# Optimization experiments

Hardware: AMD Instinct MI355X
Metric: run time of the kernel (lower is better)

Reference implementation:

```python
import jax, jax.numpy as jnp
import numpy as np

N_NODES = 100000
N_EDGES = 3200000
D = 64
NEG_SLOPE = 0.01  # torch F.leaky_relu default


def setup_inputs() -> dict:
    key = jax.random.key(0)
    ks = jax.random.split(key, 7)
    s = 1.0 / np.sqrt(D)
    x = jax.random.normal(ks[0], (N_NODES, D), jnp.float32)
    src = jax.random.randint(ks[1], (N_EDGES,), 0, N_NODES)
    dst = jax.random.randint(ks[2], (N_EDGES,), 0, N_NODES)
    W1a = jax.random.normal(ks[3], (D, D), jnp.float32) * s
    W2a = jax.random.normal(ks[4], (D, D), jnp.float32) * s
    W1b = jax.random.normal(ks[5], (D, D), jnp.float32) * s
    W2b = jax.random.normal(ks[6], (D, D), jnp.float32) * s
    return {"x": x, "W1a": W1a, "W2a": W2a, "W1b": W1b, "W2b": W2b,
            "src": src, "dst": dst}


def _ngcf_conv(x, src, dst, norm, W1, W2):
    # message: norm_ij * (W1 x_j + W2 (x_j (*) x_i)), aggregated at dst i,
    # plus self-transform W1 x_i  (NGCF propagation rule, pre-activation)
    xs = x[src]            # [E, D] gather of neighbor feats
    xd = x[dst]            # [E, D] gather of center feats
    msg = norm[:, None] * (xs @ W1 + (xs * xd) @ W2)   # [E, D]
    agg = jax.ops.segment_sum(msg, dst, num_segments=x.shape[0])
    return x @ W1 + agg


def reference(x, W1a, W2a, W1b, W2b, src, dst):
    n = x.shape[0]
    ones = jnp.ones(src.shape[0], x.dtype)
    deg = jnp.maximum(jax.ops.segment_sum(ones, dst, num_segments=n), 1.0)
    norm = jax.lax.rsqrt(deg[src] * deg[dst])          # 1/sqrt(d_j d_i)
    h1 = jax.nn.leaky_relu(_ngcf_conv(x, src, dst, norm, W1a, W2a), NEG_SLOPE)
    h2 = jax.nn.leaky_relu(_ngcf_conv(h1, src, dst, norm, W1b, W2b), NEG_SLOPE)
    h3 = _ngcf_conv(h2, src, dst, norm, W1b, W2b)      # no activation (matches source)
    return jnp.concatenate([h1, h2, h3], axis=-1)      # [N, 3*D]
```

## Files before the change

### kernel.cpp

```cpp
#include <hip/hip_runtime.h>
#include <hip/hip_bf16.h>

#define N_NODES 100000
#define N_EDGES 3200000
#define D 64
#define NEG_SLOPE 0.01f

#define B_SHIFT 9
#define NB ((N_NODES + 511) >> B_SHIFT)
#define T_EDGES 4096
#define NBIN ((N_EDGES + T_EDGES - 1) / T_EDGES)

__device__ __forceinline__ unsigned short f2bf(float f) {
    __hip_bfloat16 h = __float2bfloat16(f);
    return *reinterpret_cast<unsigned short*>(&h);
}
__device__ __forceinline__ float bflo(unsigned int u) { return __uint_as_float(u << 16); }
__device__ __forceinline__ float bfhi(unsigned int u) { return __uint_as_float(u & 0xffff0000u); }

__global__ __launch_bounds__(256) void bhist_k(const int* __restrict__ dst, int* __restrict__ btot) {
    __shared__ int hist[NB];
    int tid = threadIdx.x;
    for (int b = tid; b < NB; b += 256) hist[b] = 0;
    __syncthreads();
    int e0 = blockIdx.x * T_EDGES;
    int e1 = min(e0 + T_EDGES, N_EDGES);
    for (int e = e0 + tid; e < e1; e += 256) atomicAdd(&hist[dst[e] >> B_SHIFT], 1);
    __syncthreads();
    for (int b = tid; b < NB; b += 256) {
        int h = hist[b];
        if (h) atomicAdd(&btot[b], h);
    }
}

__global__ __launch_bounds__(256) void bscan_k(const int* __restrict__ btot, int* __restrict__ bbase) {
    __shared__ int wsum[4];
    int t = threadIdx.x;
    int lane = t & 63, w = t >> 6;
    int v = (t < NB) ? btot[t] : 0;
    int incl = v;
    #pragma unroll
    for (int o = 1; o < 64; o <<= 1) {
        int u = __shfl_up(incl, o, 64);
        if (lane >= o) incl += u;
    }
    if (lane == 63) wsum[w] = incl;
    __syncthreads();
    int woff = 0;
    for (int k = 0; k < w; ++k) woff += wsum[k];
    if (t < NB) bbase[t] = woff + incl - v;
    if (t == NB) bbase[NB] = N_EDGES;
}

__global__ __launch_bounds__(256) void bucket_k(const int* __restrict__ src, const int* __restrict__ dst,
                                                const int* __restrict__ bbase, int* __restrict__ bcnt2,
                                                int2* __restrict__ pairs) {
    __shared__ int hist[NB];
    __shared__ int lbase[NB];
    __shared__ int lcnt[NB];
    __shared__ int gbase[NB];
    __shared__ int wsum[4];
    __shared__ int2 buf[T_EDGES];
    int tid = threadIdx.x;
    for (int b = tid; b < NB; b += 256) { hist[b] = 0; lcnt[b] = 0; }
    __syncthreads();
    int e0 = blockIdx.x * T_EDGES;
    int e1 = min(e0 + T_EDGES, N_EDGES);
    for (int e = e0 + tid; e < e1; e += 256) atomicAdd(&hist[dst[e] >> B_SHIFT], 1);
    __syncthreads();
    {
        int v = (tid < NB) ? hist[tid] : 0;
        int lane = tid & 63, w = tid >> 6;
        int incl = v;
        #pragma unroll
        for (int o = 1; o < 64; o <<= 1) {
            int u = __shfl_up(incl, o, 64);
            if (lane >= o) incl += u;
        }
        if (lane == 63) wsum[w] = incl;
        __syncthreads();
        int woff = 0;
        for (int k = 0; k < w; ++k) woff += wsum[k];
        if (tid < NB) {
            int excl = woff + incl - v;
            lbase[tid] = excl;
            int p = v ? atomicAdd(&bcnt2[tid], v) : 0;
            gbase[tid] = bbase[tid] + p - excl;
        }
    }
    __syncthreads();
    for (int e = e0 + tid; e < e1; e += 256) {
        int sv = src[e], dv = dst[e];
        int b = dv >> B_SHIFT;
        int loc = lbase[b] + atomicAdd(&lcnt[b], 1);
        buf[loc] = make_int2(sv, dv);
    }
    __syncthreads();
    int n = e1 - e0;
    for (int i = tid; i < n; i += 256) {
        int2 pr = buf[i];
        int b = pr.y >> B_SHIFT;
        pairs[gbase[b] + i] = pr;
    }
}

__global__ __launch_bounds__(512) void fine_k(const int2* __restrict__ pairs, const int* __restrict__ bbase,
                                              int* __restrict__ degi, int* __restrict__ offs,
                                              float* __restrict__ rsd, int* __restrict__ csr_src) {
    __shared__ int cnt[512];
    __shared__ int offl[512];
    __shared__ int wsum[8];
    int b = blockIdx.x, t = threadIdx.x;
    int start = bbase[b];
    int end = bbase[b + 1];
    cnt[t] = 0;
    __syncthreads();
    for (int e = start + t; e < end; e += 512) atomicAdd(&cnt[pairs[e].y & 511], 1);
    __syncthreads();
    int d = cnt[t];
    int lane = t & 63, w = t >> 6;
    int incl = d;
    #pragma unroll
    for (int o = 1; o < 64; o <<= 1) {
        int u = __shfl_up(incl, o, 64);
        if (lane >= o) incl += u;
    }
    if (lane == 63) wsum[w] = incl;
    __syncthreads();
    int woff = 0;
    for (int k = 0; k < w; ++k) woff += wsum[k];
    int myoff = start + woff + incl - d;
    offl[t] = myoff;
    int n = (b << B_SHIFT) + t;
    if (n < N_NODES) {
        degi[n] = d;
        offs[n] = myoff;
        rsd[n] = rsqrtf((float)(d > 0 ? d : 1));
    }
    cnt[t] = 0;
    __syncthreads();
    for (int e = start + t; e < end; e += 512) {
        int2 pr = pairs[e];
        int li = pr.y & 511;
        int p = atomicAdd(&cnt[li], 1);
        csr_src[offl[li] + p] = pr.x;
    }
}

__global__ __launch_bounds__(256) void cvt_k(const float* __restrict__ x, const float* __restrict__ rsd,
                                             unsigned short* __restrict__ xb) {
    int i = blockIdx.x * 256 + threadIdx.x;
    if (i < N_NODES * 16) {
        int node = i >> 4;
        float rn = rsd[node];
        float4 v = ((const float4*)x)[i];
        unsigned int lo = ((unsigned int)f2bf(rn * v.y) << 16) | f2bf(rn * v.x);
        unsigned int hi = ((unsigned int)f2bf(rn * v.w) << 16) | f2bf(rn * v.z);
        ((uint2*)xb)[i] = make_uint2(lo, hi);
    }
}

__global__ __launch_bounds__(256) void agg_k(const unsigned short* __restrict__ xb,
                                             const float* __restrict__ rsd,
                                             const int* __restrict__ offs, const int* __restrict__ degi,
                                             const int* __restrict__ csr_src, float* __restrict__ s) {
    int node = blockIdx.x * 4 + (threadIdx.x >> 6);
    if (node >= N_NODES) return;
    int lane = threadIdx.x & 63;
    int g = lane >> 3;
    int q = lane & 7;
    int start = offs[node];
    int deg = degi[node];
    const uint4* in4 = (const uint4*)xb;
    float acc0 = 0.f, acc1 = 0.f, acc2 = 0.f, acc3 = 0.f;
    float acc4 = 0.f, acc5 = 0.f, acc6 = 0.f, acc7 = 0.f;
    for (int base = 0; base < deg; base += 64) {
        int m = min(deg - base, 64);
        int idxv = csr_src[start + base + min(lane, m - 1)];
        for (int j = 0; j < m; j += 32) {
            int e0 = j + g, e1 = j + 8 + g, e2 = j + 16 + g, e3 = j + 24 + g;
            bool v0 = e0 < m, v1 = e1 < m, v2 = e2 < m, v3 = e3 < m;
            int s0 = __shfl(idxv, e0, 64);
            int s1 = __shfl(idxv, v1 ? e1 : 0, 64);
            int s2 = __shfl(idxv, v2 ? e2 : 0, 64);
            int s3 = __shfl(idxv, v3 ? e3 : 0, 64);
            uint4 p0 = in4[(size_t)s0 * 8 + q];
            uint4 p1 = in4[(size_t)s1 * 8 + q];
            uint4 p2 = in4[(size_t)s2 * 8 + q];
            uint4 p3 = in4[(size_t)s3 * 8 + q];
            float w0 = v0 ? 1.f : 0.f, w1 = v1 ? 1.f : 0.f;
            float w2 = v2 ? 1.f : 0.f, w3 = v3 ? 1.f : 0.f;
            acc0 += w0 * bflo(p0.x); acc1 += w0 * bfhi(p0.x);
            acc2 += w0 * bflo(p0.y); acc3 += w0 * bfhi(p0.y);
            acc4 += w0 * bflo(p0.z); acc5 += w0 * bfhi(p0.z);
            acc6 += w0 * bflo(p0.w); acc7 += w0 * bfhi(p0.w);
            acc0 += w1 * bflo(p1.x); acc1 += w1 * bfhi(p1.x);
            acc2 += w1 * bflo(p1.y); acc3 += w1 * bfhi(p1.y);
            acc4 += w1 * bflo(p1.z); acc5 += w1 * bfhi(p1.z);
            acc6 += w1 * bflo(p1.w); acc7 += w1 * bfhi(p1.w);
            acc0 += w2 * bflo(p2.x); acc1 += w2 * bfhi(p2.x);
            acc2 += w2 * bflo(p2.y); acc3 += w2 * bfhi(p2.y);
            acc4 += w2 * bflo(p2.z); acc5 += w2 * bfhi(p2.z);
            acc6 += w2 * bflo(p2.w); acc7 += w2 * bfhi(p2.w);
            acc0 += w3 * bflo(p3.x); acc1 += w3 * bfhi(p3.x);
            acc2 += w3 * bflo(p3.y); acc3 += w3 * bfhi(p3.y);
            acc4 += w3 * bflo(p3.z); acc5 += w3 * bfhi(p3.z);
            acc6 += w3 * bflo(p3.w); acc7 += w3 * bfhi(p3.w);
        }
    }
    #pragma unroll
    for (int off = 8; off < 64; off <<= 1) {
        acc0 += __shfl_xor(acc0, off, 64); acc1 += __shfl_xor(acc1, off, 64);
        acc2 += __shfl_xor(acc2, off, 64); acc3 += __shfl_xor(acc3, off, 64);
        acc4 += __shfl_xor(acc4, off, 64); acc5 += __shfl_xor(acc5, off, 64);
        acc6 += __shfl_xor(acc6, off, 64); acc7 += __shfl_xor(acc7, off, 64);
    }
    if (g == 0) {
        float rn = rsd[node];
        float4 r0, r1;
        r0.x = rn * acc0; r0.y = rn * acc1; r0.z = rn * acc2; r0.w = rn * acc3;
        r1.x = rn * acc4; r1.y = rn * acc5; r1.z = rn * acc6; r1.w = rn * acc7;
        ((float4*)s)[node * 16 + q * 2]     = r0;
        ((float4*)s)[node * 16 + q * 2 + 1] = r1;
    }
}

__global__ __launch_bounds__(256) void comb_k(const float* __restrict__ in, int stride,
                                              const float* __restrict__ s,
                                              const float* __restrict__ W1, const float* __restrict__ W2,
                                              float* __restrict__ out, int act,
                                              unsigned short* __restrict__ hb, const float* __restrict__ rsd,
                                              int bfout) {
    __shared__ float W1s[D * D];
    __shared__ float W2s[D * D];
    __shared__ float aL[4][4][D];
    __shared__ float bL[4][4][D];
    int tid = threadIdx.x;
    {
        const float4* w1v = (const float4*)W1;
        const float4* w2v = (const float4*)W2;
        float4* w1s = (float4*)W1s;
        float4* w2s = (float4*)W2s;
        for (int t = tid; t < D * D / 4; t += 256) { w1s[t] = w1v[t]; w2s[t] = w2v[t]; }
    }
    int w = tid >> 6;
    int l = tid & 63;
    int m = l >> 4;
    int cb = (l & 15) * 4;
    __syncthreads();
    for (int it = 0; it < 2; ++it) {
        int n0 = blockIdx.x * 32 + it * 16 + w * 4;
        #pragma unroll
        for (int mm = 0; mm < 4; ++mm) {
            float xv = in[(size_t)(n0 + mm) * stride + l];
            float sp = s[(size_t)(n0 + mm) * D + l];
            aL[w][mm][l] = xv + sp;
            bL[w][mm][l] = sp * xv;
        }
        __syncthreads();
        float acc0 = 0.f, acc1 = 0.f, acc2 = 0.f, acc3 = 0.f;
        const float4* aV = (const float4*)&aL[w][m][0];
        const float4* bV = (const float4*)&bL[w][m][0];
        #pragma unroll
        for (int kk = 0; kk < 16; ++kk) {
            float4 a4 = aV[kk];
            float4 b4 = bV[kk];
            #pragma unroll
            for (int j = 0; j < 4; ++j) {
                int k = kk * 4 + j;
                float aj = (j == 0) ? a4.x : (j == 1) ? a4.y : (j == 2) ? a4.z : a4.w;
                float bj = (j == 0) ? b4.x : (j == 1) ? b4.y : (j == 2) ? b4.z : b4.w;
                float4 w1 = *(const float4*)&W1s[k * D + cb];
                float4 w2 = *(const float4*)&W2s[k * D + cb];
                acc0 += aj * w1.x + bj * w2.x;
                acc1 += aj * w1.y + bj * w2.y;
                acc2 += aj * w1.z + bj * w2.z;
                acc3 += aj * w1.w + bj * w2.w;
            }
        }
        int n = n0 + m;
        float4 r;
        r.x = acc0; r.y = acc1; r.z = acc2; r.w = acc3;
        if (act) {
            r.x = r.x >= 0.f ? r.x : NEG_SLOPE * r.x;
            r.y = r.y >= 0.f ? r.y : NEG_SLOPE * r.y;
            r.z = r.z >= 0.f ? r.z : NEG_SLOPE * r.z;
            r.w = r.w >= 0.f ? r.w : NEG_SLOPE * r.w;
        }
        *(float4*)&out[(size_t)n * 192 + cb] = r;
        if (bfout) {
            float rn = rsd[n];
            unsigned int lo = ((unsigned int)f2bf(rn * r.y) << 16) | f2bf(rn * r.x);
            unsigned int hi = ((unsigned int)f2bf(rn * r.w) << 16) | f2bf(rn * r.z);
            *(uint2*)&hb[(size_t)n * D + cb] = make_uint2(lo, hi);
        }
        __syncthreads();
    }
}

extern "C" void kernel_launch(void* const* d_in, const int* in_sizes, int n_in,
                              void* d_out, int out_size, void* d_ws, size_t ws_size,
                              hipStream_t stream) {
    const float* x   = (const float*)d_in[0];
    const float* W1a = (const float*)d_in[1];
    const float* W2a = (const float*)d_in[2];
    const float* W1b = (const float*)d_in[3];
    const float* W2b = (const float*)d_in[4];
    const int*   src = (const int*)d_in[5];
    const int*   dst = (const int*)d_in[6];
    float* out = (float*)d_out;

    int*   btot    = (int*)d_ws;
    int*   bcnt2   = btot + 256;
    int*   bbase   = bcnt2 + 256;
    int*   degi    = bbase + 256;
    int*   offs    = degi + N_NODES;
    float* rsd     = (float*)(offs + N_NODES);
    int*   csr_src = (int*)(rsd + N_NODES);
    int2*  pairs   = (int2*)(csr_src + N_EDGES);
    unsigned short* xb = (unsigned short*)pairs;
    unsigned short* hb = xb + (size_t)N_NODES * D;
    float* s       = (float*)(pairs + N_EDGES);

    hipMemsetAsync(btot, 0, 512 * sizeof(int), stream);

    bhist_k<<<NBIN, 256, 0, stream>>>(dst, btot);
    bscan_k<<<1, 256, 0, stream>>>(btot, bbase);
    bucket_k<<<NBIN, 256, 0, stream>>>(src, dst, bbase, bcnt2, pairs);
    fine_k<<<NB, 512, 0, stream>>>(pairs, bbase, degi, offs, rsd, csr_src);
    cvt_k<<<(N_NODES * 16 + 255) / 256, 256, 0, stream>>>(x, rsd, xb);

    int ab = (N_NODES + 3) / 4;
    int cbg = N_NODES / 32;

    agg_k<<<ab, 256, 0, stream>>>(xb, rsd, offs, degi, csr_src, s);
    comb_k<<<cbg, 256, 0, stream>>>(x, D, s, W1a, W2a, out + 0, 1, hb, rsd, 1);
    agg_k<<<ab, 256, 0, stream>>>(hb, rsd, offs, degi, csr_src, s);
    comb_k<<<cbg, 256, 0, stream>>>(out + 0, 192, s, W1b, W2b, out + 64, 1, hb, rsd, 1);
    agg_k<<<ab, 256, 0, stream>>>(hb, rsd, offs, degi, csr_src, s);
    comb_k<<<cbg, 256, 0, stream>>>(out + 64, 192, s, W1b, W2b, out + 128, 0, hb, rsd, 0);
}
```

Baseline: 534.1 us.

## Use split-bf16 MFMA for the combine GEMM instead of FP32 FMA loops

The combine kernel's dense 64x64 transforms are rewritten to use bf16 MFMA 16x16x32 instructions. Each operand is split into a high and a low bf16 part, and three products per weight matrix approximate FP32 accuracy. Weights are loaded straight into registers per wave, which drops the shared-memory staging and the block barriers. In exchange the kernel issues extra conversion arithmetic, and its outputs become scattered scalar stores instead of float4 stores.

```diff
diff --git a/kernel.cpp b/kernel.cpp
--- a/kernel.cpp
+++ b/kernel.cpp
@@ -11,12 +11,16 @@
 #define T_EDGES 4096
 #define NBIN ((N_EDGES + T_EDGES - 1) / T_EDGES)
 
+using bf16x8 = __attribute__((ext_vector_type(8))) short;
+using f32x4  = __attribute__((ext_vector_type(4))) float;
+
 __device__ __forceinline__ unsigned short f2bf(float f) {
     __hip_bfloat16 h = __float2bfloat16(f);
     return *reinterpret_cast<unsigned short*>(&h);
 }
 __device__ __forceinline__ float bflo(unsigned int u) { return __uint_as_float(u << 16); }
 __device__ __forceinline__ float bfhi(unsigned int u) { return __uint_as_float(u & 0xffff0000u); }
+__device__ __forceinline__ float bf2f(unsigned short h) { return __uint_as_float(((unsigned int)h) << 16); }
 
 __global__ __launch_bounds__(256) void bhist_k(const int* __restrict__ dst, int* __restrict__ btot) {
     __shared__ int hist[NB];
@@ -231,70 +235,77 @@
                                               float* __restrict__ out, int act,
                                               unsigned short* __restrict__ hb, const float* __restrict__ rsd,
                                               int bfout) {
-    __shared__ float W1s[D * D];
-    __shared__ float W2s[D * D];
-    __shared__ float aL[4][4][D];
-    __shared__ float bL[4][4][D];
     int tid = threadIdx.x;
-    {
-        const float4* w1v = (const float4*)W1;
-        const float4* w2v = (const float4*)W2;
-        float4* w1s = (float4*)W1s;
-        float4* w2s = (float4*)W2s;
-        for (int t = tid; t < D * D / 4; t += 256) { w1s[t] = w1v[t]; w2s[t] = w2v[t]; }
-    }
     int w = tid >> 6;
     int l = tid & 63;
-    int m = l >> 4;
-    int cb = (l & 15) * 4;
-    __syncthreads();
-    for (int it = 0; it < 2; ++it) {
-        int n0 = blockIdx.x * 32 + it * 16 + w * 4;
-        #pragma unroll
-        for (int mm = 0; mm < 4; ++mm) {
-            float xv = in[(size_t)(n0 + mm) * stride + l];
-            float sp = s[(size_t)(n0 + mm) * D + l];
-            aL[w][mm][l] = xv + sp;
-            bL[w][mm][l] = sp * xv;
-        }
-        __syncthreads();
-        float acc0 = 0.f, acc1 = 0.f, acc2 = 0.f, acc3 = 0.f;
-        const float4* aV = (const float4*)&aL[w][m][0];
-        const float4* bV = (const float4*)&bL[w][m][0];
-        #pragma unroll
-        for (int kk = 0; kk < 16; ++kk) {
-            float4 a4 = aV[kk];
-            float4 b4 = bV[kk];
+    int lr = l & 15;
+    int lk = l >> 4;
+
+    bf16x8 w1h[2], w1l[2], w2h[2], w2l[2];
+    #pragma unroll
+    for (int s2 = 0; s2 < 2; ++s2) {
+        #pragma unroll
+        for (int i = 0; i < 8; ++i) {
+            int k = s2 * 32 + lk * 8 + i;
+            float v1 = W1[k * D + w * 16 + lr];
+            float v2 = W2[k * D + w * 16 + lr];
+            unsigned short h1 = f2bf(v1);
+            unsigned short h2 = f2bf(v2);
+            w1h[s2][i] = (short)h1; w1l[s2][i] = (short)f2bf(v1 - bf2f(h1));
+            w2h[s2][i] = (short)h2; w2l[s2][i] = (short)f2bf(v2 - bf2f(h2));
+        }
+    }
+
+    int n0 = blockIdx.x * 32;
+    bf16x8 ah[2][2], al[2][2], bh[2][2], bl[2][2];
+    #pragma unroll
+    for (int rt = 0; rt < 2; ++rt) {
+        int n = n0 + rt * 16 + lr;
+        const float* ip = in + (size_t)n * stride + lk * 8;
+        const float* sp = s + (size_t)n * D + lk * 8;
+        #pragma unroll
+        for (int s2 = 0; s2 < 2; ++s2) {
+            float ia[8], sa[8];
+            *(float4*)&ia[0] = *(const float4*)(ip + s2 * 32);
+            *(float4*)&ia[4] = *(const float4*)(ip + s2 * 32 + 4);
+            *(float4*)&sa[0] = *(const float4*)(sp + s2 * 32);
+            *(float4*)&sa[4] = *(const float4*)(sp + s2 * 32 + 4);
             #pragma unroll
-            for (int j = 0; j < 4; ++j) {
-                int k = kk * 4 + j;
-                float aj = (j == 0) ? a4.x : (j == 1) ? a4.y : (j == 2) ? a4.z : a4.w;
-                float bj = (j == 0) ? b4.x : (j == 1) ? b4.y : (j == 2) ? b4.z : b4.w;
-                float4 w1 = *(const float4*)&W1s[k * D + cb];
-                float4 w2 = *(const float4*)&W2s[k * D + cb];
-                acc0 += aj * w1.x + bj * w2.x;
-                acc1 += aj * w1.y + bj * w2.y;
-                acc2 += aj * w1.z + bj * w2.z;
-                acc3 += aj * w1.w + bj * w2.w;
+            for (int i = 0; i < 8; ++i) {
+                float a = ia[i] + sa[i];
+                float b = sa[i] * ia[i];
+                unsigned short hA = f2bf(a);
+                unsigned short hB = f2bf(b);
+                ah[rt][s2][i] = (short)hA; al[rt][s2][i] = (short)f2bf(a - bf2f(hA));
+                bh[rt][s2][i] = (short)hB; bl[rt][s2][i] = (short)f2bf(b - bf2f(hB));
             }
         }
-        int n = n0 + m;
-        float4 r;
-        r.x = acc0; r.y = acc1; r.z = acc2; r.w = acc3;
-        if (act) {
-            r.x = r.x >= 0.f ? r.x : NEG_SLOPE * r.x;
-            r.y = r.y >= 0.f ? r.y : NEG_SLOPE * r.y;
-            r.z = r.z >= 0.f ? r.z : NEG_SLOPE * r.z;
-            r.w = r.w >= 0.f ? r.w : NEG_SLOPE * r.w;
-        }
-        *(float4*)&out[(size_t)n * 192 + cb] = r;
-        if (bfout) {
-            float rn = rsd[n];
-            unsigned int lo = ((unsigned int)f2bf(rn * r.y) << 16) | f2bf(rn * r.x);
-            unsigned int hi = ((unsigned int)f2bf(rn * r.w) << 16) | f2bf(rn * r.z);
-            *(uint2*)&hb[(size_t)n * D + cb] = make_uint2(lo, hi);
-        }
-        __syncthreads();
+    }
+
+    f32x4 acc[2] = {{0.f, 0.f, 0.f, 0.f}, {0.f, 0.f, 0.f, 0.f}};
+    #pragma unroll
+    for (int rt = 0; rt < 2; ++rt) {
+        #pragma unroll
+        for (int s2 = 0; s2 < 2; ++s2) {
+            acc[rt] = __builtin_amdgcn_mfma_f32_16x16x32_bf16(ah[rt][s2], w1h[s2], acc[rt], 0, 0, 0);
+            acc[rt] = __builtin_amdgcn_mfma_f32_16x16x32_bf16(al[rt][s2], w1h[s2], acc[rt], 0, 0, 0);
+            acc[rt] = __builtin_amdgcn_mfma_f32_16x16x32_bf16(ah[rt][s2], w1l[s2], acc[rt], 0, 0, 0);
+            acc[rt] = __builtin_amdgcn_mfma_f32_16x16x32_bf16(bh[rt][s2], w2h[s2], acc[rt], 0, 0, 0);
+            acc[rt] = __builtin_amdgcn_mfma_f32_16x16x32_bf16(bl[rt][s2], w2h[s2], acc[rt], 0, 0, 0);
+            acc[rt] = __builtin_amdgcn_mfma_f32_16x16x32_bf16(bh[rt][s2], w2l[s2], acc[rt], 0, 0, 0);
+        }
+    }
+
+    #pragma unroll
+    for (int rt = 0; rt < 2; ++rt) {
+        #pragma unroll
+        for (int r = 0; r < 4; ++r) {
+            int n = n0 + rt * 16 + lk * 4 + r;
+            float v = acc[rt][r];
+            if (act) v = v >= 0.f ? v : NEG_SLOPE * v;
+            out[(size_t)n * 192 + w * 16 + lr] = v;
+            if (bfout) hb[(size_t)n * D + w * 16 + lr] = f2bf(rsd[n] * v);
+        }
     }
 }
 
```

Result: faster. 461.3 us (-13.6%).
